# Optimization experiments

Measured on AMD Instinct MI355X. Metric: run time of the kernel, lower is better.

## Reference

```python
import jax, jax.numpy as jnp
import numpy as np

B, Q, HID = 2, 1024, 2048
NH, NKV, HD = 32, 8, 64          # num heads, kv heads, head_dim (HID = NH*HD)
GROUPS = NH // NKV
KB_N, TOPK = 512, 100            # kb entries, top_k_kb
KB_MAX_TRAIN = 512               # kb_max_train_triples (kb_length_scaling=True)
ROPE_THETA = 10000.0


def rotate_half(x):
    x1, x2 = jnp.split(x, 2, axis=-1)
    return jnp.concatenate([-x2, x1], axis=-1)


def setup_inputs() -> dict:
    key = jax.random.key(0)
    ks = jax.random.split(key, 10)
    sc = 1.0 / np.sqrt(HID)
    hidden_states = jax.random.normal(ks[0], (B, Q, HID), jnp.float32)
    kb_kvs = jax.random.normal(ks[1], (B, KB_N, HID), jnp.float32)
    Wq = jax.random.normal(ks[2], (HID, NH * HD), jnp.float32) * sc
    Wk = jax.random.normal(ks[3], (HID, NKV * HD), jnp.float32) * sc
    Wv = jax.random.normal(ks[4], (HID, NKV * HD), jnp.float32) * sc
    Wo = jax.random.normal(ks[5], (NH * HD, HID), jnp.float32) * sc
    Wq_new = jax.random.normal(ks[6], (HID, NH * HD), jnp.float32) * sc
    Wkb_k = jax.random.normal(ks[7], (HID, NKV * HD), jnp.float32) * sc
    Wkb_v = jax.random.normal(ks[8], (HID, NKV * HD), jnp.float32) * sc
    # RoPE tables [Q, HD]
    inv_freq = 1.0 / (ROPE_THETA ** (jnp.arange(0, HD, 2, dtype=jnp.float32) / HD))
    t = jnp.arange(Q, dtype=jnp.float32)
    freqs = t[:, None] * inv_freq[None, :]
    emb = jnp.concatenate([freqs, freqs], axis=-1)
    cos, sin = jnp.cos(emb), jnp.sin(emb)
    position_ids = jnp.broadcast_to(jnp.arange(Q), (B, Q))
    # additive causal mask [B,1,Q,Q]
    i = jnp.arange(Q)
    causal = jnp.where(i[None, :] <= i[:, None], 0.0, -1e9).astype(jnp.float32)
    attention_mask = jnp.broadcast_to(causal[None, None], (B, 1, Q, Q))
    return dict(hidden_states=hidden_states, kb_kvs=kb_kvs, Wq=Wq, Wk=Wk, Wv=Wv,
                Wo=Wo, Wq_new=Wq_new, Wkb_k=Wkb_k, Wkb_v=Wkb_v, cos=cos, sin=sin,
                attention_mask=attention_mask, position_ids=position_ids)


def attention_fwd(hidden_states, kb_kvs, Wq, Wk, Wv, Wo, Wq_new, Wkb_k, Wkb_v,
                  cos, sin, attention_mask, position_ids):
    b, q_len, _ = hidden_states.shape
    q = (hidden_states @ Wq).reshape(b, q_len, NH, HD).transpose(0, 2, 1, 3)
    k = (hidden_states @ Wk).reshape(b, q_len, NKV, HD).transpose(0, 2, 1, 3)
    v = (hidden_states @ Wv).reshape(b, q_len, NKV, HD).transpose(0, 2, 1, 3)
    # RoPE
    c = cos[position_ids][:, None]  # [b,1,q,hd]
    s = sin[position_ids][:, None]
    q = q * c + rotate_half(q) * s
    k = k * c + rotate_half(k) * s
    # repeat_kv (GQA expansion)
    k = jnp.repeat(k, GROUPS, axis=1)
    v = jnp.repeat(v, GROUPS, axis=1)
    # KB branch (layer_idx=0, kb_layer_index=0 -> slice is full hidden dim)
    kb_k = (kb_kvs @ Wkb_k).reshape(b, KB_N, NKV, HD).transpose(0, 2, 1, 3)
    kb_v = (kb_kvs @ Wkb_v).reshape(b, KB_N, NKV, HD).transpose(0, 2, 1, 3)
    kb_k = jnp.repeat(kb_k, GROUPS, axis=1)
    kb_v = jnp.repeat(kb_v, GROUPS, axis=1)
    kb_q = (hidden_states @ Wq_new).reshape(b, q_len, NH, HD).transpose(0, 2, 1, 3)
    scale = 1.0 / jnp.sqrt(jnp.float32(HD))
    aw_kb = jnp.einsum('bhqd,bhkd->bhqk', kb_q, kb_k) * scale  # [b,nh,q,KB_N]
    # top-k KB entry selection (scores summed over heads and query positions)
    sel_scores = aw_kb.sum(axis=(1, 2))                        # [b,KB_N]
    _, top_idx = jax.lax.top_k(sel_scores, TOPK)               # [b,TOPK]
    kb_v = jnp.take_along_axis(kb_v, top_idx[:, None, :, None], axis=2)
    aw_kb = jnp.take_along_axis(aw_kb, top_idx[:, None, None, :], axis=3)
    # kb length scaling: log(max_train_triples) - log(current kb len)
    aw_kb = aw_kb + (jnp.log(jnp.float32(KB_MAX_TRAIN)) - jnp.log(jnp.float32(TOPK)))
    aw_p = jnp.einsum('bhqd,bhkd->bhqk', q, k) * scale + attention_mask
    aw = jax.nn.softmax(jnp.concatenate([aw_kb, aw_p], axis=-1).astype(jnp.float32), axis=-1)
    aw = aw.astype(q.dtype)
    cv = jnp.concatenate([kb_v, v], axis=2)                    # [b,nh,TOPK+q,hd]
    out = jnp.einsum('bhqk,bhkd->bhqd', aw, cv)
    out = out.transpose(0, 2, 1, 3).reshape(b, q_len, NH * HD)
    return out @ Wo


def reference(hidden_states, kb_kvs, Wq, Wk, Wv, Wo, Wq_new, Wkb_k, Wkb_v,
              cos, sin, attention_mask, position_ids):
    return attention_fwd(hidden_states, kb_kvs, Wq, Wk, Wv, Wo, Wq_new, Wkb_k,
                         Wkb_v, cos, sin, attention_mask, position_ids)
```

## Files before the change

### kernel.cpp

```cpp
#include <hip/hip_runtime.h>

typedef unsigned short u16;
typedef unsigned int   u32;
typedef __bf16 bf16_t;
typedef bf16_t bf16x8 __attribute__((ext_vector_type(8)));
typedef float  floatx4 __attribute__((ext_vector_type(4)));

#define B_    2
#define QS    1024
#define HID_  2048
#define NH_   32
#define NKV_  8
#define HD_   64
#define KBN_  512
#define TOPK_ 100
#define FS    5120

__device__ __forceinline__ float b2f(u16 u) {
  union { u32 i; float f; } x; x.i = ((u32)u) << 16; return x.f;
}
__device__ __forceinline__ u16 f2b(float f) {
  union { float f; u32 i; } x; x.f = f;
  u32 r = x.i + 0x7fffu + ((x.i >> 16) & 1u);
  return (u16)(r >> 16);
}
__device__ __forceinline__ void async16(const u16* g, u16* l) {
  __builtin_amdgcn_global_load_lds(
      (const __attribute__((address_space(1))) unsigned int*)g,
      (__attribute__((address_space(3))) unsigned int*)l, 16, 0, 0);
}

__global__ __launch_bounds__(256)
void tc7_k(const float* __restrict__ Wq, const float* __restrict__ Wk,
           const float* __restrict__ Wv, const float* __restrict__ Wqn,
           const float* __restrict__ Wkbk, const float* __restrict__ Wkbv,
           const float* __restrict__ Wo, u16* __restrict__ WT,
           u16* __restrict__ WTkb, u16* __restrict__ WTo,
           const float* __restrict__ hs, const float* __restrict__ kb,
           u16* __restrict__ hsb, u16* __restrict__ kbb,
           double* __restrict__ partH) {
  int id = blockIdx.x, t = threadIdx.x;
  if (id >= 22528) {
    int l = id - 22528;
    int qc = l & 63, b = l >> 6;
    double a[8] = {0, 0, 0, 0, 0, 0, 0, 0};
    for (int qq = 0; qq < 16; ++qq) {
      const float* row = hs + (size_t)(b * QS + qc * 16 + qq) * HID_;
#pragma unroll
      for (int m = 0; m < 8; ++m) a[m] += (double)row[m * 256 + t];
    }
#pragma unroll
    for (int m = 0; m < 8; ++m)
      partH[(size_t)qc * (B_ * HID_) + b * HID_ + m * 256 + t] = a[m];
    return;
  }
  if (id >= 16384) {
    const float* x; u16* y; int j;
    if (id < 20480) { x = hs; y = hsb; j = (id - 16384) * 256 + t; }
    else            { x = kb; y = kbb; j = (id - 20480) * 256 + t; }
    float4 v = ((const float4*)x)[j];
    ((uint2*)y)[j] = make_uint2((u32)f2b(v.x) | ((u32)f2b(v.y) << 16),
                                (u32)f2b(v.z) | ((u32)f2b(v.w) << 16));
    return;
  }
  const float* W; u16* D; int N, bx, by;
  if (id < 4096)       { W = Wq;   D = WT;                        N = 2048; int l = id;         bx = l & 63; by = l >> 6; }
  else if (id < 5120)  { W = Wk;   D = WT + (size_t)2048 * 2048;  N = 512;  int l = id - 4096;  bx = l & 15; by = l >> 4; }
  else if (id < 6144)  { W = Wv;   D = WT + (size_t)2560 * 2048;  N = 512;  int l = id - 5120;  bx = l & 15; by = l >> 4; }
  else if (id < 10240) { W = Wqn;  D = WT + (size_t)3072 * 2048;  N = 2048; int l = id - 6144;  bx = l & 63; by = l >> 6; }
  else if (id < 11264) { W = Wkbk; D = WTkb;                      N = 512;  int l = id - 10240; bx = l & 15; by = l >> 4; }
  else if (id < 12288) { W = Wkbv; D = WTkb + (size_t)512 * 2048; N = 512;  int l = id - 11264; bx = l & 15; by = l >> 4; }
  else                 { W = Wo;   D = WTo;                       N = 2048; int l = id - 12288; bx = l & 63; by = l >> 6; }
  const int K = 2048;
  __shared__ float tile[32][33];
  int n0 = bx * 32, k0 = by * 32;
  int tx = t & 31, ty = t >> 5;
#pragma unroll
  for (int i = 0; i < 32; i += 8)
    tile[ty + i][tx] = W[(size_t)(k0 + ty + i) * N + n0 + tx];
  __syncthreads();
#pragma unroll
  for (int i = 0; i < 32; i += 8)
    D[(size_t)(n0 + ty + i) * K + k0 + tx] = f2b(tile[tx][ty + i]);
}

__global__ __launch_bounds__(512, 2)
void gemm256j(const u16* __restrict__ A0, const u16* __restrict__ B0,
              u16* __restrict__ C0, const u16* __restrict__ A1,
              const u16* __restrict__ B1, u16* __restrict__ C1, int K,
              const double* __restrict__ partH, const float* __restrict__ Wqn,
              double* __restrict__ partS) {
  __shared__ __align__(16) u16 sm[65536];
  const int tid = threadIdx.x, lane = tid & 63, w = tid >> 6;
  int orig = blockIdx.x;
  if (orig >= 176) {
    int l = orig - 176;
    int chunk = l & 127, b = l >> 7, j = tid;
    double* tmpd = (double*)sm;
    double* hsl  = tmpd + 1024;
    int g = j >> 6, d = j & 63;
    int c0 = chunk * 16;
    {
      int ch = j >> 4, cc = j & 15;
      tmpd[ch * 16 + cc]        = partH[(size_t)ch * (B_ * HID_) + b * HID_ + c0 + cc];
      tmpd[(ch + 32) * 16 + cc] = partH[(size_t)(ch + 32) * (B_ * HID_) + b * HID_ + c0 + cc];
    }
    __syncthreads();
    if (j < 16) {
      double a = 0.0;
      for (int ch = 0; ch < 64; ++ch) a += tmpd[ch * 16 + j];
      hsl[j] = a;
    }
    __syncthreads();
    double acc = 0.0;
    for (int cc = 0; cc < 16; ++cc) {
      int c = c0 + cc;
      const float* wq = Wqn + (size_t)c * HID_ + g * 256 + d;
      acc += hsl[cc] *
             ((double)wq[0] + (double)wq[64] + (double)wq[128] + (double)wq[192]);
    }
    partS[(size_t)chunk * (B_ * 512) + b * 512 + j] = acc;
    return;
  }
  const int wr = w >> 2, wc = w & 3;
  int swz = (orig & 7) * 22 + (orig >> 3);
  const u16 *A, *BT; u16* C; int CS, bx, by;
  if (swz < 160) { A = A0; BT = B0; C = C0; CS = FS;   bx = swz % 20; by = swz / 20; }
  else { int t2 = swz - 160; A = A1; BT = B1; C = C1; CS = 1024; bx = t2 & 3; by = t2 >> 2; }
  int m0 = by << 8, n0 = bx << 8;
  const int NT = K >> 6;

  int lr = lane >> 2;
  int colsw = ((lane & 3) * 8) ^ ((lane & 32) ? 16 : 0);
  const u16* gA[2][2]; const u16* gB[2][2];
  int lA[2][2];
#pragma unroll
  for (int h = 0; h < 2; ++h)
#pragma unroll
    for (int j = 0; j < 2; ++j) {
      int ij = 2 * w + j, kk = ij >> 3, rb = (ij & 7) * 16;
      gA[h][j] = A + (size_t)(m0 + h * 128 + rb + lr) * K + kk * 32 + colsw;
      gB[h][j] = BT + (size_t)(n0 + h * 128 + rb + lr) * K + kk * 32 + colsw;
      lA[h][j] = kk * 8192 + (h * 128 + rb) * 32;
    }
  int fsw = ((lane >> 4) * 8) ^ ((lane & 8) ? 16 : 0);
  int aoff = (wr * 128 + (lane & 15)) * 32 + fsw;
  int boff = 16384 + (wc * 64 + (lane & 15)) * 32 + fsw;

  floatx4 acc[8][4];
#pragma unroll
  for (int i = 0; i < 8; ++i)
#pragma unroll
    for (int j = 0; j < 4; ++j) acc[i][j] = (floatx4){0.f, 0.f, 0.f, 0.f};
  bf16x8 a[4][2], b[4][2];

#define STG_(g, l, u) async16((g) + (size_t)(u) * 64, &sm[(((u) & 1) << 15) + (l)])
#define BAR_ do { asm volatile("" ::: "memory"); __builtin_amdgcn_s_barrier(); \
                  asm volatile("" ::: "memory"); } while (0)
#define LG0_ do { asm volatile("s_waitcnt lgkmcnt(0)" ::: "memory"); \
                  __builtin_amdgcn_sched_barrier(0); } while (0)

  STG_(gA[0][0], lA[0][0], 0); STG_(gA[0][1], lA[0][1], 0);
  STG_(gA[1][0], lA[1][0], 0); STG_(gA[1][1], lA[1][1], 0);
  STG_(gB[0][0], lA[0][0] + 16384, 0); STG_(gB[0][1], lA[0][1] + 16384, 0);
  STG_(gB[1][0], lA[1][0] + 16384, 0); STG_(gB[1][1], lA[1][1] + 16384, 0);
  if (NT > 1) {
    STG_(gB[0][0], lA[0][0] + 16384, 1); STG_(gB[0][1], lA[0][1] + 16384, 1);
    STG_(gA[0][0], lA[0][0], 1); STG_(gA[0][1], lA[0][1], 1);
    asm volatile("s_waitcnt vmcnt(4)" ::: "memory");
  } else {
    asm volatile("s_waitcnt vmcnt(0)" ::: "memory");
  }
  BAR_;

  for (int u = 0; u < NT; ++u) {
    const int cb = (u & 1) << 15;
#pragma unroll
    for (int kk = 0; kk < 2; ++kk) {
#pragma unroll
      for (int mi = 0; mi < 4; ++mi)
        a[mi][kk] = *(const bf16x8*)&sm[cb + kk * 8192 + aoff + mi * 512];
#pragma unroll
      for (int ni = 0; ni < 2; ++ni)
        b[ni][kk] = *(const bf16x8*)&sm[cb + kk * 8192 + boff + ni * 512];
    }
    if (u + 1 < NT) { STG_(gA[1][0], lA[1][0], u + 1); STG_(gA[1][1], lA[1][1], u + 1); }
    BAR_; LG0_;
    __builtin_amdgcn_s_setprio(1);
#pragma unroll
    for (int mi = 0; mi < 4; ++mi)
#pragma unroll
      for (int ni = 0; ni < 2; ++ni)
#pragma unroll
        for (int kk = 0; kk < 2; ++kk)
          acc[mi][ni] = __builtin_amdgcn_mfma_f32_16x16x32_bf16(
              a[mi][kk], b[ni][kk], acc[mi][ni], 0, 0, 0);
    __builtin_amdgcn_s_setprio(0);
    BAR_;
#pragma unroll
    for (int kk = 0; kk < 2; ++kk)
#pragma unroll
      for (int ni = 0; ni < 2; ++ni)
        b[2 + ni][kk] = *(const bf16x8*)&sm[cb + kk * 8192 + boff + (2 + ni) * 512];
    if (u + 1 < NT) { STG_(gB[1][0], lA[1][0] + 16384, u + 1);
                      STG_(gB[1][1], lA[1][1] + 16384, u + 1); }
    BAR_; LG0_;
    __builtin_amdgcn_s_setprio(1);
#pragma unroll
    for (int mi = 0; mi < 4; ++mi)
#pragma unroll
      for (int ni = 0; ni < 2; ++ni)
#pragma unroll
        for (int kk = 0; kk < 2; ++kk)
          acc[mi][2 + ni] = __builtin_amdgcn_mfma_f32_16x16x32_bf16(
              a[mi][kk], b[2 + ni][kk], acc[mi][2 + ni], 0, 0, 0);
    __builtin_amdgcn_s_setprio(0);
    BAR_;
#pragma unroll
    for (int kk = 0; kk < 2; ++kk)
#pragma unroll
      for (int mi = 0; mi < 4; ++mi)
        a[mi][kk] = *(const bf16x8*)&sm[cb + kk * 8192 + aoff + 2048 + mi * 512];
    if (u + 2 < NT) { STG_(gB[0][0], lA[0][0] + 16384, u + 2);
                      STG_(gB[0][1], lA[0][1] + 16384, u + 2); }
    BAR_; LG0_;
    __builtin_amdgcn_s_setprio(1);
#pragma unroll
    for (int mi = 0; mi < 4; ++mi)
#pragma unroll
      for (int ni = 0; ni < 2; ++ni)
#pragma unroll
        for (int kk = 0; kk < 2; ++kk)
          acc[4 + mi][2 + ni] = __builtin_amdgcn_mfma_f32_16x16x32_bf16(
              a[mi][kk], b[2 + ni][kk], acc[4 + mi][2 + ni], 0, 0, 0);
    __builtin_amdgcn_s_setprio(0);
    BAR_;
    if (u + 2 < NT) {
      STG_(gA[0][0], lA[0][0], u + 2); STG_(gA[0][1], lA[0][1], u + 2);
      asm volatile("s_waitcnt vmcnt(4)" ::: "memory");
    } else {
      asm volatile("s_waitcnt vmcnt(0)" ::: "memory");
    }
    BAR_;
    __builtin_amdgcn_s_setprio(1);
#pragma unroll
    for (int mi = 0; mi < 4; ++mi)
#pragma unroll
      for (int ni = 0; ni < 2; ++ni)
#pragma unroll
        for (int kk = 0; kk < 2; ++kk)
          acc[4 + mi][ni] = __builtin_amdgcn_mfma_f32_16x16x32_bf16(
              a[mi][kk], b[ni][kk], acc[4 + mi][ni], 0, 0, 0);
    __builtin_amdgcn_s_setprio(0);
    BAR_;
  }
#undef STG_
#undef BAR_
#undef LG0_
  int quad = lane >> 4, col = lane & 15;
#pragma unroll
  for (int mi = 0; mi < 8; ++mi)
#pragma unroll
    for (int ni = 0; ni < 4; ++ni)
#pragma unroll
      for (int rr = 0; rr < 4; ++rr)
        C[(size_t)(m0 + wr * 128 + mi * 16 + quad * 4 + rr) * CS +
          n0 + wc * 64 + ni * 16 + col] = f2b(acc[mi][ni][rr]);
}

__global__ __launch_bounds__(512, 2)
void gemm256s(const u16* __restrict__ A, const u16* __restrict__ BT,
              float* __restrict__ Out, int N, int LDK, int Kl, int ntiles) {
  __shared__ __align__(16) u16 sm[65536];
  const int tid = threadIdx.x, lane = tid & 63, w = tid >> 6;
  const int wr = w >> 2, wc = w & 3;
  const int nbx = N >> 8;
  int nwg = gridDim.x, orig = blockIdx.x, swz = orig;
  if ((nwg & 7) == 0) swz = (orig & 7) * (nwg >> 3) + (orig >> 3);
  int tile = swz % ntiles, slice = swz / ntiles;
  int bx = tile % nbx, by = tile / nbx;
  int m0 = by << 8, n0 = bx << 8;
  const int NT = Kl >> 6;
  const u16* As = A + (size_t)slice * Kl;
  const u16* Bs = BT + (size_t)slice * Kl;

  int lr = lane >> 2;
  int colsw = ((lane & 3) * 8) ^ ((lane & 32) ? 16 : 0);
  const u16* gA[2][2]; const u16* gB[2][2];
  int lA[2][2];
#pragma unroll
  for (int h = 0; h < 2; ++h)
#pragma unroll
    for (int j = 0; j < 2; ++j) {
      int ij = 2 * w + j, kk = ij >> 3, rb = (ij & 7) * 16;
      gA[h][j] = As + (size_t)(m0 + h * 128 + rb + lr) * LDK + kk * 32 + colsw;
      gB[h][j] = Bs + (size_t)(n0 + h * 128 + rb + lr) * LDK + kk * 32 + colsw;
      lA[h][j] = kk * 8192 + (h * 128 + rb) * 32;
    }
  int fsw = ((lane >> 4) * 8) ^ ((lane & 8) ? 16 : 0);
  int aoff = (wr * 128 + (lane & 15)) * 32 + fsw;
  int boff = 16384 + (wc * 64 + (lane & 15)) * 32 + fsw;

  floatx4 acc[8][4];
#pragma unroll
  for (int i = 0; i < 8; ++i)
#pragma unroll
    for (int j = 0; j < 4; ++j) acc[i][j] = (floatx4){0.f, 0.f, 0.f, 0.f};
  bf16x8 a[4][2], b[4][2];

#define STG_(g, l, u) async16((g) + (size_t)(u) * 64, &sm[(((u) & 1) << 15) + (l)])
#define BAR_ do { asm volatile("" ::: "memory"); __builtin_amdgcn_s_barrier(); \
                  asm volatile("" ::: "memory"); } while (0)
#define LG0_ do { asm volatile("s_waitcnt lgkmcnt(0)" ::: "memory"); \
                  __builtin_amdgcn_sched_barrier(0); } while (0)

  STG_(gA[0][0], lA[0][0], 0); STG_(gA[0][1], lA[0][1], 0);
  STG_(gA[1][0], lA[1][0], 0); STG_(gA[1][1], lA[1][1], 0);
  STG_(gB[0][0], lA[0][0] + 16384, 0); STG_(gB[0][1], lA[0][1] + 16384, 0);
  STG_(gB[1][0], lA[1][0] + 16384, 0); STG_(gB[1][1], lA[1][1] + 16384, 0);
  if (NT > 1) {
    STG_(gB[0][0], lA[0][0] + 16384, 1); STG_(gB[0][1], lA[0][1] + 16384, 1);
    STG_(gA[0][0], lA[0][0], 1); STG_(gA[0][1], lA[0][1], 1);
    asm volatile("s_waitcnt vmcnt(4)" ::: "memory");
  } else {
    asm volatile("s_waitcnt vmcnt(0)" ::: "memory");
  }
  BAR_;

  for (int u = 0; u < NT; ++u) {
    const int cb = (u & 1) << 15;
#pragma unroll
    for (int kk = 0; kk < 2; ++kk) {
#pragma unroll
      for (int mi = 0; mi < 4; ++mi)
        a[mi][kk] = *(const bf16x8*)&sm[cb + kk * 8192 + aoff + mi * 512];
#pragma unroll
      for (int ni = 0; ni < 2; ++ni)
        b[ni][kk] = *(const bf16x8*)&sm[cb + kk * 8192 + boff + ni * 512];
    }
    if (u + 1 < NT) { STG_(gA[1][0], lA[1][0], u + 1); STG_(gA[1][1], lA[1][1], u + 1); }
    BAR_; LG0_;
    __builtin_amdgcn_s_setprio(1);
#pragma unroll
    for (int mi = 0; mi < 4; ++mi)
#pragma unroll
      for (int ni = 0; ni < 2; ++ni)
#pragma unroll
        for (int kk = 0; kk < 2; ++kk)
          acc[mi][ni] = __builtin_amdgcn_mfma_f32_16x16x32_bf16(
              a[mi][kk], b[ni][kk], acc[mi][ni], 0, 0, 0);
    __builtin_amdgcn_s_setprio(0);
    BAR_;
#pragma unroll
    for (int kk = 0; kk < 2; ++kk)
#pragma unroll
      for (int ni = 0; ni < 2; ++ni)
        b[2 + ni][kk] = *(const bf16x8*)&sm[cb + kk * 8192 + boff + (2 + ni) * 512];
    if (u + 1 < NT) { STG_(gB[1][0], lA[1][0] + 16384, u + 1);
                      STG_(gB[1][1], lA[1][1] + 16384, u + 1); }
    BAR_; LG0_;
    __builtin_amdgcn_s_setprio(1);
#pragma unroll
    for (int mi = 0; mi < 4; ++mi)
#pragma unroll
      for (int ni = 0; ni < 2; ++ni)
#pragma unroll
        for (int kk = 0; kk < 2; ++kk)
          acc[mi][2 + ni] = __builtin_amdgcn_mfma_f32_16x16x32_bf16(
              a[mi][kk], b[2 + ni][kk], acc[mi][2 + ni], 0, 0, 0);
    __builtin_amdgcn_s_setprio(0);
    BAR_;
#pragma unroll
    for (int kk = 0; kk < 2; ++kk)
#pragma unroll
      for (int mi = 0; mi < 4; ++mi)
        a[mi][kk] = *(const bf16x8*)&sm[cb + kk * 8192 + aoff + 2048 + mi * 512];
    if (u + 2 < NT) { STG_(gB[0][0], lA[0][0] + 16384, u + 2);
                      STG_(gB[0][1], lA[0][1] + 16384, u + 2); }
    BAR_; LG0_;
    __builtin_amdgcn_s_setprio(1);
#pragma unroll
    for (int mi = 0; mi < 4; ++mi)
#pragma unroll
      for (int ni = 0; ni < 2; ++ni)
#pragma unroll
        for (int kk = 0; kk < 2; ++kk)
          acc[4 + mi][2 + ni] = __builtin_amdgcn_mfma_f32_16x16x32_bf16(
              a[mi][kk], b[2 + ni][kk], acc[4 + mi][2 + ni], 0, 0, 0);
    __builtin_amdgcn_s_setprio(0);
    BAR_;
    if (u + 2 < NT) {
      STG_(gA[0][0], lA[0][0], u + 2); STG_(gA[0][1], lA[0][1], u + 2);
      asm volatile("s_waitcnt vmcnt(4)" ::: "memory");
    } else {
      asm volatile("s_waitcnt vmcnt(0)" ::: "memory");
    }
    BAR_;
    __builtin_amdgcn_s_setprio(1);
#pragma unroll
    for (int mi = 0; mi < 4; ++mi)
#pragma unroll
      for (int ni = 0; ni < 2; ++ni)
#pragma unroll
        for (int kk = 0; kk < 2; ++kk)
          acc[4 + mi][ni] = __builtin_amdgcn_mfma_f32_16x16x32_bf16(
              a[mi][kk], b[ni][kk], acc[4 + mi][ni], 0, 0, 0);
    __builtin_amdgcn_s_setprio(0);
    BAR_;
  }
#undef STG_
#undef BAR_
#undef LG0_
  int quad = lane >> 4, col = lane & 15;
#pragma unroll
  for (int mi = 0; mi < 8; ++mi)
#pragma unroll
    for (int ni = 0; ni < 4; ++ni)
#pragma unroll
      for (int rr = 0; rr < 4; ++rr)
        unsafeAtomicAdd(&Out[(size_t)(m0 + wr * 128 + mi * 16 + quad * 4 + rr) * N +
                             n0 + wc * 64 + ni * 16 + col], acc[mi][ni][rr]);
}

__global__ __launch_bounds__(256)
void rv_k(u16* __restrict__ fused, const float* __restrict__ ct,
          const float* __restrict__ st, const int* __restrict__ pid,
          u16* __restrict__ vt, const double* __restrict__ partS,
          const float* __restrict__ Wkbk, double* __restrict__ partU) {
  __shared__ __align__(16) char rsm[33792];
  int bid = blockIdx.x, t = threadIdx.x;
  if (bid < 10240) {
    int gid = bid * 256 + t;
    const int nq = B_ * QS * NH_ * 32;
    u16* x; int nh, g2;
    if (gid < nq) { x = fused;        nh = NH_;  g2 = gid; }
    else          { x = fused + 2048; nh = NKV_; g2 = gid - nq; }
    int per_row = nh * 32;
    int row = g2 / per_row;
    int rem = g2 - row * per_row;
    int h = rem >> 5, d = rem & 31;
    int pos = pid[row];
    float c = ct[pos * 64 + d];
    float s = st[pos * 64 + d];
    size_t base = (size_t)row * FS + h * 64 + d;
    float x0 = b2f(x[base]), x1 = b2f(x[base + 32]);
    x[base]      = f2b(x0 * c - x1 * s);
    x[base + 32] = f2b(x1 * c + x0 * s);
    return;
  }
  if (bid >= 10496) {
    int l = bid - 10496;
    int jc = l & 3, yy = l >> 2;
    int b = yy >> 3;
    int c = (yy & 7) * 256 + t;
    double* buf = (double*)rsm;
    double* Sl  = (double*)(rsm + 32768);
    double a = 0.0;
    for (int pass = 0; pass < 4; ++pass) {
      int chb = pass * 32;
#pragma unroll
      for (int e = t; e < 4096; e += 256) {
        int ch = e >> 7, jj = e & 127;
        buf[ch * 128 + jj] = partS[(size_t)(chb + ch) * (B_ * 512) + b * 512 + jc * 128 + jj];
      }
      __syncthreads();
      if (t < 128) {
        for (int ch = 0; ch < 32; ++ch) a += buf[ch * 128 + t];
      }
      __syncthreads();
    }
    if (t < 128) Sl[t] = a;
    __syncthreads();
    const float* row = Wkbk + (size_t)c * 512 + jc * 128;
    double acc = 0.0;
    for (int j = 0; j < 128; j += 4) {
      float4 wv = *(const float4*)(row + j);
      acc += Sl[j] * (double)wv.x + Sl[j + 1] * (double)wv.y +
             Sl[j + 2] * (double)wv.z + Sl[j + 3] * (double)wv.w;
    }
    partU[(size_t)jc * (B_ * HID_) + b * HID_ + c] = acc;
    return;
  }
  int l = bid - 10240;
  int kt = l & 15, bg = l >> 4;
  int b = bg >> 3, g = bg & 7;
  u16* tile = (u16*)rsm;
  {
    int kk = t >> 2, dc = (t & 3) * 16;
    const u16* src = fused + (size_t)(b * QS + kt * 64 + kk) * FS + 2560 + g * 64 + dc;
    *(uint4*)&tile[kk * 72 + dc]     = *(const uint4*)src;
    *(uint4*)&tile[kk * 72 + dc + 8] = *(const uint4*)(src + 8);
  }
  __syncthreads();
  {
    int d = t >> 2, kc = t & 3;
    __align__(16) u16 tmp[16];
#pragma unroll
    for (int i = 0; i < 16; ++i) tmp[i] = tile[(kc * 16 + i) * 72 + d];
    u16* dst = vt + ((size_t)bg * 64 + d) * 1024 + kt * 64 + kc * 16;
    *(uint4*)dst       = *(uint4*)&tmp[0];
    *(uint4*)(dst + 8) = *(uint4*)&tmp[8];
  }
}

__global__ __launch_bounds__(256)
void self2_k(const double* __restrict__ partU, const float* __restrict__ kbin,
             double* __restrict__ part) {
  int n = blockIdx.x * 256 + threadIdx.x;
  int cc = blockIdx.y, b = blockIdx.z;
  int t = threadIdx.x;
  __shared__ double ul[256];
  {
    size_t ui = (size_t)b * HID_ + cc * 256 + t;
    double a = partU[ui];
    a += partU[(size_t)(B_ * HID_) + ui];
    a += partU[2 * (size_t)(B_ * HID_) + ui];
    a += partU[3 * (size_t)(B_ * HID_) + ui];
    ul[t] = a;
  }
  __syncthreads();
  const float* row = kbin + (size_t)(b * KBN_ + n) * HID_ + cc * 256;
  double acc = 0.0;
  for (int c = 0; c < 256; c += 4) {
    float4 kv = *(const float4*)(row + c);
    acc += ul[c] * (double)kv.x + ul[c + 1] * (double)kv.y +
           ul[c + 2] * (double)kv.z + ul[c + 3] * (double)kv.w;
  }
  part[(size_t)cc * (B_ * KBN_) + b * KBN_ + n] = acc;
}

__global__ __launch_bounds__(512)
void topk_rank_k(const double* __restrict__ partSel, int* __restrict__ idx) {
  int b = blockIdx.x, i = threadIdx.x;
  __shared__ float v[KBN_];
  double a = 0.0;
#pragma unroll
  for (int c = 0; c < 8; ++c) a += partSel[(size_t)c * (B_ * KBN_) + b * KBN_ + i];
  float vi = (float)a;
  v[i] = vi;
  __syncthreads();
  int rank = 0;
#pragma unroll 8
  for (int j = 0; j < KBN_; ++j) {
    float vj = v[j];
    rank += (vj > vi || (vj == vi && j < i)) ? 1 : 0;
  }
  if (rank < TOPK_) idx[b * TOPK_ + rank] = i;
}

__global__ __launch_bounds__(256)
void kbgather_k(const u16* __restrict__ kbf, const int* __restrict__ topidx,
                u16* __restrict__ kbt) {
  int bg = blockIdx.x; int b = bg >> 3, g = bg & 7;
  int t = threadIdx.x;
  int d = t >> 2, s0 = (t & 3) * 32;
  __align__(16) u16 tmp[32];
#pragma unroll
  for (int i = 0; i < 32; ++i) {
    int slot = s0 + i;
    int n = topidx[b * TOPK_ + (slot < TOPK_ ? slot : TOPK_ - 1)];
    tmp[i] = kbf[(size_t)(b * KBN_ + n) * 1024 + 512 + g * 64 + d];
  }
  u16* dst = kbt + ((size_t)bg * 64 + d) * 128 + s0;
#pragma unroll
  for (int i = 0; i < 32; i += 8) *(uint4*)(dst + i) = *(uint4*)&tmp[i];
}

__global__ __launch_bounds__(256)
void attn_mfma_k(const u16* __restrict__ fused, const u16* __restrict__ kbf,
                 const u16* __restrict__ vt, const u16* __restrict__ kbt,
                 const int* __restrict__ topidx, u16* __restrict__ ctx) {
  int bid = blockIdx.x;
  int raw = bid >> 6;
  int hb = bid & 63;
  int h = hb & 31, b = hb >> 5;
  int pg = raw >> 2, pp = raw & 3;
  int pbase = (pg >> 1) * 4 + pp;
  int qt = (pg & 1) ? (15 - pbase) : pbase;
  int g = h >> 2;
  int t = threadIdx.x, lane = t & 63, w = t >> 6;
  int quad = lane >> 4, col = lane & 15;
  __shared__ __align__(16) u16 ks[64 * 72];
  __shared__ __align__(16) u16 vst[64 * 64];
  __shared__ __align__(16) u16 ps[4][16 * 72];
  const float LOGADJ = 1.6331544f;
  int q0 = qt * 64;

  int qrow_frag = q0 + w * 16 + col;
  bf16x8 aKB[2], aC[2];
#pragma unroll
  for (int kstep = 0; kstep < 2; ++kstep) {
    const u16* p1 = fused + (size_t)(b * QS + qrow_frag) * FS + 3072 + h * 64 + kstep * 32 + quad * 8;
    const u16* p2 = fused + (size_t)(b * QS + qrow_frag) * FS + 0    + h * 64 + kstep * 32 + quad * 8;
    uint4 x1 = *(const uint4*)p1, x2 = *(const uint4*)p2;
    const u16* u1 = (const u16*)&x1; const u16* u2 = (const u16*)&x2;
#pragma unroll
    for (int i = 0; i < 8; ++i) {
      aKB[kstep][i] = (bf16_t)(0.125f * b2f(u1[i]));
      aC[kstep][i]  = (bf16_t)(0.125f * b2f(u2[i]));
    }
  }

  float mrow[4] = {-1e30f, -1e30f, -1e30f, -1e30f};
  float lrow[4] = {0.f, 0.f, 0.f, 0.f};
  floatx4 acc[4];
#pragma unroll
  for (int nb = 0; nb < 4; ++nb) acc[nb] = (floatx4){0.f, 0.f, 0.f, 0.f};

  int sj = t >> 2, sdc = (t & 3) * 16, sc4 = t & 3;
  uint4 kr0, kr1, vr0, vr1;

#define LOADTILE(TT) do {                                                      \
    int _t = (TT);                                                             \
    const u16 *_src, *_vsrc;                                                   \
    if (_t < 2) {                                                              \
      int _slot = _t * 64 + sj;                                                \
      int _n = topidx[b * TOPK_ + (_slot < TOPK_ ? _slot : TOPK_ - 1)];        \
      _src = kbf + (size_t)(b * KBN_ + _n) * 1024 + g * 64 + sdc;              \
      _vsrc = kbt + ((size_t)(b * 8 + g) * 64 + sj) * 128 + _t * 64 + sc4 * 16;\
    } else {                                                                   \
      int _key = (_t - 2) * 64 + sj;                                           \
      _src = fused + (size_t)(b * QS + _key) * FS + 2048 + g * 64 + sdc;       \
      _vsrc = vt + ((size_t)(b * 8 + g) * 64 + sj) * 1024 + (_t - 2) * 64 + sc4 * 16; \
    }                                                                          \
    kr0 = *(const uint4*)_src;  kr1 = *(const uint4*)(_src + 8);               \
    vr0 = *(const uint4*)_vsrc; vr1 = *(const uint4*)(_vsrc + 8);              \
  } while (0)

  int ntiles = 2 + (q0 >> 6) + 1;
  LOADTILE(0);
  for (int tile = 0; tile < ntiles; ++tile) {
    __syncthreads();
    *(uint4*)&ks[sj * 72 + sdc]     = kr0;
    *(uint4*)&ks[sj * 72 + sdc + 8] = kr1;
    {
      int sw = sj & 7;
      *(uint4*)&vst[sj * 64 + ((2 * sc4)     ^ sw) * 8] = vr0;
      *(uint4*)&vst[sj * 64 + ((2 * sc4 + 1) ^ sw) * 8] = vr1;
    }
    if (tile + 1 < ntiles) LOADTILE(tile + 1);
    __syncthreads();

    bf16x8 aq0 = (tile < 2) ? aKB[0] : aC[0];
    bf16x8 aq1 = (tile < 2) ? aKB[1] : aC[1];
    floatx4 s[4];
#pragma unroll
    for (int nb = 0; nb < 4; ++nb) {
      s[nb] = (floatx4){0.f, 0.f, 0.f, 0.f};
      bf16x8 b0 = *(bf16x8*)&ks[(nb * 16 + col) * 72 + quad * 8];
      bf16x8 b1 = *(bf16x8*)&ks[(nb * 16 + col) * 72 + 32 + quad * 8];
      s[nb] = __builtin_amdgcn_mfma_f32_16x16x32_bf16(aq0, b0, s[nb], 0, 0, 0);
      s[nb] = __builtin_amdgcn_mfma_f32_16x16x32_bf16(aq1, b1, s[nb], 0, 0, 0);
    }
    if (tile < 2) {
      if (tile == 0) {
#pragma unroll
        for (int nb = 0; nb < 4; ++nb)
#pragma unroll
          for (int rr = 0; rr < 4; ++rr) s[nb][rr] += LOGADJ;
      } else {
#pragma unroll
        for (int nb = 0; nb < 4; ++nb) {
          bool dead = (64 + nb * 16 + col) >= TOPK_;
#pragma unroll
          for (int rr = 0; rr < 4; ++rr)
            s[nb][rr] = dead ? -1e30f : (s[nb][rr] + LOGADJ);
        }
      }
    } else if (tile == ntiles - 1) {
      int kbase = (tile - 2) * 64;
#pragma unroll
      for (int nb = 0; nb < 4; ++nb) {
        int key = kbase + nb * 16 + col;
#pragma unroll
        for (int rr = 0; rr < 4; ++rr) {
          int qrow = q0 + w * 16 + quad * 4 + rr;
          if (key > qrow) s[nb][rr] = -1e30f;
        }
      }
    }
    float tm[4];
#pragma unroll
    for (int rr = 0; rr < 4; ++rr)
      tm[rr] = fmaxf(fmaxf(s[0][rr], s[1][rr]), fmaxf(s[2][rr], s[3][rr]));
#pragma unroll
    for (int off = 1; off < 16; off <<= 1)
#pragma unroll
      for (int rr = 0; rr < 4; ++rr)
        tm[rr] = fmaxf(tm[rr], __shfl_xor(tm[rr], off));
    float alpha[4], rs[4];
#pragma unroll
    for (int rr = 0; rr < 4; ++rr) {
      float mn = fmaxf(mrow[rr], tm[rr]);
      alpha[rr] = __expf(mrow[rr] - mn);
      mrow[rr] = mn;
      rs[rr] = 0.f;
    }
#pragma unroll
    for (int nb = 0; nb < 4; ++nb)
#pragma unroll
      for (int rr = 0; rr < 4; ++rr) {
        float ev = __expf(s[nb][rr] - mrow[rr]);
        rs[rr] += ev;
        ps[w][(quad * 4 + rr) * 72 + nb * 16 + col] = f2b(ev);
      }
#pragma unroll
    for (int off = 1; off < 16; off <<= 1)
#pragma unroll
      for (int rr = 0; rr < 4; ++rr)
        rs[rr] += __shfl_xor(rs[rr], off);
#pragma unroll
    for (int rr = 0; rr < 4; ++rr) lrow[rr] = lrow[rr] * alpha[rr] + rs[rr];
#pragma unroll
    for (int nb = 0; nb < 4; ++nb)
#pragma unroll
      for (int rr = 0; rr < 4; ++rr) acc[nb][rr] *= alpha[rr];

    bf16x8 pa0 = *(bf16x8*)&ps[w][col * 72 + quad * 8];
    bf16x8 pa1 = *(bf16x8*)&ps[w][col * 72 + 32 + quad * 8];
#pragma unroll
    for (int nb = 0; nb < 4; ++nb) {
      int d = nb * 16 + col;
      int sw = (d & 7) << 3;
      bf16x8 vb0 = *(bf16x8*)&vst[d * 64 + ((quad * 8) ^ sw)];
      bf16x8 vb1 = *(bf16x8*)&vst[d * 64 + ((32 + quad * 8) ^ sw)];
      acc[nb] = __builtin_amdgcn_mfma_f32_16x16x32_bf16(pa0, vb0, acc[nb], 0, 0, 0);
      acc[nb] = __builtin_amdgcn_mfma_f32_16x16x32_bf16(pa1, vb1, acc[nb], 0, 0, 0);
    }
  }
#undef LOADTILE
#pragma unroll
  for (int rr = 0; rr < 4; ++rr) {
    float inv = 1.f / lrow[rr];
    int qrow = q0 + w * 16 + quad * 4 + rr;
    size_t base = (size_t)(b * QS + qrow) * HID_ + h * 64;
#pragma unroll
    for (int nb = 0; nb < 4; ++nb)
      ctx[base + nb * 16 + col] = f2b(acc[nb][rr] * inv);
  }
}

extern "C" void kernel_launch(void* const* d_in, const int* in_sizes, int n_in,
                              void* d_out, int out_size, void* d_ws, size_t ws_size,
                              hipStream_t stream) {
  (void)in_sizes; (void)n_in; (void)out_size; (void)ws_size;
  const float* hs_f = (const float*)d_in[0];
  const float* kb_f = (const float*)d_in[1];
  const float* Wq   = (const float*)d_in[2];
  const float* Wk   = (const float*)d_in[3];
  const float* Wv   = (const float*)d_in[4];
  const float* Wo   = (const float*)d_in[5];
  const float* Wqn  = (const float*)d_in[6];
  const float* Wkbk = (const float*)d_in[7];
  const float* Wkbv = (const float*)d_in[8];
  const float* cosT = (const float*)d_in[9];
  const float* sinT = (const float*)d_in[10];
  const int*   pid  = (const int*)d_in[12];
  float* out = (float*)d_out;

  char* p = (char*)d_ws;
  u16* WT    = (u16*)p; p += (size_t)FS * 2048 * 2;
  u16* WTkb  = (u16*)p; p += (size_t)1024 * 2048 * 2;
  u16* WTo   = (u16*)p; p += (size_t)2048 * 2048 * 2;
  u16* fused = (u16*)p; p += (size_t)B_ * QS * FS * 2;
  u16* hs_b  = (u16*)p; p += (size_t)B_ * QS * HID_ * 2;
  u16* kb_b  = (u16*)p; p += (size_t)B_ * KBN_ * HID_ * 2;
  u16* kbf   = (u16*)p; p += (size_t)B_ * KBN_ * 1024 * 2;
  int*    idx_ws   = (int*)p;    p += (size_t)B_ * TOPK_ * 4 + 4;
  double* partH    = (double*)p; p += (size_t)64 * B_ * HID_ * 8;
  double* partS    = (double*)p; p += (size_t)128 * B_ * 512 * 8;
  double* partU    = (double*)p; p += (size_t)4 * B_ * HID_ * 8;
  double* partSel  = (double*)p; p += (size_t)8 * B_ * KBN_ * 8;
  u16* ctx_ws = hs_b;
  u16* v_t    = kb_b;
  u16* kb_t   = kb_b + (size_t)B_ * 8 * 64 * 1024;

  dim3 blk(256);
  hipMemsetAsync(out, 0, (size_t)2048 * 2048 * 4, stream);
  tc7_k<<<dim3(22656), blk, 0, stream>>>(Wq, Wk, Wv, Wqn, Wkbk, Wkbv, Wo,
                                         WT, WTkb, WTo, hs_f, kb_f, hs_b, kb_b, partH);
  gemm256j<<<dim3(432), dim3(512), 0, stream>>>(hs_b, WT, fused, kb_b, WTkb, kbf, 2048,
                                                partH, Wqn, partS);
  rv_k<<<dim3(10560), blk, 0, stream>>>(fused, cosT, sinT, pid, v_t,
                                        partS, Wkbk, partU);
  self2_k<<<dim3(2, 8, B_), blk, 0, stream>>>(partU, kb_f, partSel);
  topk_rank_k<<<dim3(B_), dim3(512), 0, stream>>>(partSel, idx_ws);
  kbgather_k<<<dim3(B_ * 8), blk, 0, stream>>>(kbf, idx_ws, kb_t);
  attn_mfma_k<<<dim3(16 * NH_ * B_), blk, 0, stream>>>(fused, kbf, v_t, kb_t, idx_ws, ctx_ws);
  gemm256s<<<dim3(64 * 4), dim3(512), 0, stream>>>(ctx_ws, WTo, out, 2048, 2048, 512, 64);
}
```

Before: 393.7 us.

## Replace split-K atomic adds with partial buffers and last-block reduction

The split-K output projection GEMM now writes each K-slice's fp32 partial tile to a workspace buffer instead of doing atomic adds into the output. A per-tile counter picks the last-arriving block, which sums all slices with float4 loads and writes the output directly. This removes the output memset and the atomic traffic, but adds extra global writes and reads of partials (4 slices × 16 MB) and a serialized reduction tail in one block per tile.

```diff
diff --git a/kernel.cpp b/kernel.cpp
--- a/kernel.cpp
+++ b/kernel.cpp
@@ -270,6 +270,7 @@
 
 __global__ __launch_bounds__(512, 2)
 void gemm256s(const u16* __restrict__ A, const u16* __restrict__ BT,
+              float* __restrict__ P, int* __restrict__ cnt,
               float* __restrict__ Out, int N, int LDK, int Kl, int ntiles) {
   __shared__ __align__(16) u16 sm[65536];
   const int tid = threadIdx.x, lane = tid & 63, w = tid >> 6;
@@ -278,6 +279,7 @@
   int nwg = gridDim.x, orig = blockIdx.x, swz = orig;
   if ((nwg & 7) == 0) swz = (orig & 7) * (nwg >> 3) + (orig >> 3);
   int tile = swz % ntiles, slice = swz / ntiles;
+  const int nslice = nwg / ntiles;
   int bx = tile % nbx, by = tile / nbx;
   int m0 = by << 8, n0 = bx << 8;
   const int NT = Kl >> 6;
@@ -412,14 +414,36 @@
 #undef BAR_
 #undef LG0_
   int quad = lane >> 4, col = lane & 15;
+  const size_t ss = (size_t)ntiles << 16;
+  float* Pp = P + (size_t)slice * ss;
 #pragma unroll
   for (int mi = 0; mi < 8; ++mi)
 #pragma unroll
     for (int ni = 0; ni < 4; ++ni)
 #pragma unroll
       for (int rr = 0; rr < 4; ++rr)
-        unsafeAtomicAdd(&Out[(size_t)(m0 + wr * 128 + mi * 16 + quad * 4 + rr) * N +
-                             n0 + wc * 64 + ni * 16 + col], acc[mi][ni][rr]);
+        Pp[(size_t)(m0 + wr * 128 + mi * 16 + quad * 4 + rr) * N +
+           n0 + wc * 64 + ni * 16 + col] = acc[mi][ni][rr];
+  __threadfence();
+  __syncthreads();
+  __shared__ int windone;
+  if (tid == 0)
+    windone = (atomicAdd(&cnt[tile], 1) == nslice - 1) ? 1 : 0;
+  __syncthreads();
+  if (!windone) return;
+  __threadfence();
+  int r0 = tid >> 2, c0 = (tid & 3) * 64;
+  for (int pass = 0; pass < 2; ++pass) {
+    size_t base = (size_t)(m0 + r0 + pass * 128) * N + n0 + c0;
+    for (int i = 0; i < 64; i += 4) {
+      float4 av = *(const float4*)&P[base + i];
+      for (int s = 1; s < nslice; ++s) {
+        float4 bv = *(const float4*)&P[(size_t)s * ss + base + i];
+        av.x += bv.x; av.y += bv.y; av.z += bv.z; av.w += bv.w;
+      }
+      *(float4*)&Out[base + i] = av;
+    }
+  }
 }
 
 __global__ __launch_bounds__(256)
@@ -766,17 +790,19 @@
   u16* hs_b  = (u16*)p; p += (size_t)B_ * QS * HID_ * 2;
   u16* kb_b  = (u16*)p; p += (size_t)B_ * KBN_ * HID_ * 2;
   u16* kbf   = (u16*)p; p += (size_t)B_ * KBN_ * 1024 * 2;
-  int*    idx_ws   = (int*)p;    p += (size_t)B_ * TOPK_ * 4 + 4;
   double* partH    = (double*)p; p += (size_t)64 * B_ * HID_ * 8;
   double* partS    = (double*)p; p += (size_t)128 * B_ * 512 * 8;
   double* partU    = (double*)p; p += (size_t)4 * B_ * HID_ * 8;
   double* partSel  = (double*)p; p += (size_t)8 * B_ * KBN_ * 8;
+  float*  partKG   = (float*)p;  p += (size_t)4 * 2048 * 2048 * 4;
+  int*    idx_ws   = (int*)p;    p += 1024;
+  int*    cnt_ws   = (int*)p;    p += 64 * 4;
   u16* ctx_ws = hs_b;
   u16* v_t    = kb_b;
   u16* kb_t   = kb_b + (size_t)B_ * 8 * 64 * 1024;
 
   dim3 blk(256);
-  hipMemsetAsync(out, 0, (size_t)2048 * 2048 * 4, stream);
+  hipMemsetAsync(cnt_ws, 0, 64 * sizeof(int), stream);
   tc7_k<<<dim3(22656), blk, 0, stream>>>(Wq, Wk, Wv, Wqn, Wkbk, Wkbv, Wo,
                                          WT, WTkb, WTo, hs_f, kb_f, hs_b, kb_b, partH);
   gemm256j<<<dim3(432), dim3(512), 0, stream>>>(hs_b, WT, fused, kb_b, WTkb, kbf, 2048,
@@ -787,5 +813,6 @@
   topk_rank_k<<<dim3(B_), dim3(512), 0, stream>>>(partSel, idx_ws);
   kbgather_k<<<dim3(B_ * 8), blk, 0, stream>>>(kbf, idx_ws, kb_t);
   attn_mfma_k<<<dim3(16 * NH_ * B_), blk, 0, stream>>>(fused, kbf, v_t, kb_t, idx_ws, ctx_ws);
-  gemm256s<<<dim3(64 * 4), dim3(512), 0, stream>>>(ctx_ws, WTo, out, 2048, 2048, 512, 64);
-}
+  gemm256s<<<dim3(64 * 4), dim3(512), 0, stream>>>(ctx_ws, WTo, partKG, cnt_ws, out,
+                                                   2048, 2048, 512, 64);
+}
```

Measured after the change: 550.7 us. 39.9% more time.
